# Kernel optimization log

Measured on AMD Instinct MI355X. Metric: run time of the kernel, lower is better.

The kernel has to match this reference:

```python
import jax, jax.numpy as jnp
from jax import lax
import numpy as np

T, B, D, H, A = 512, 2048, 64, 64, 16  # time, batch, input_dim, hidden_size, action_dim


def setup_inputs() -> dict:
    key = jax.random.key(0)
    ks = jax.random.split(key, 7)
    s = 1.0 / np.sqrt(H)  # PyTorch LSTMCell/Linear init scale
    return {
        "x": jax.random.normal(ks[0], (T, B, D), dtype=jnp.float32),
        "W_ih": jax.random.uniform(ks[1], (4 * H, D), jnp.float32, -s, s),
        "W_hh": jax.random.uniform(ks[2], (4 * H, H), jnp.float32, -s, s),
        "b_ih": jax.random.uniform(ks[3], (4 * H,), jnp.float32, -s, s),
        "b_hh": jax.random.uniform(ks[4], (4 * H,), jnp.float32, -s, s),
        "W_out": jax.random.uniform(ks[5], (A, H), jnp.float32, -s, s),
        "b_out": jax.random.uniform(ks[6], (A,), jnp.float32, -s, s),
    }


def reference(x, W_ih, W_hh, b_ih, b_hh, W_out, b_out):
    # x: [T, B, D]; single-layer LSTMCell unrolled over time via lax.scan,
    # zero initial (h, c) as in init_hidden_state(batch_size=B).
    Bh = x.shape[1]
    Hd = W_hh.shape[1]
    bias = b_ih + b_hh  # fuse the two biases

    def step(carry, x_t):
        h, c = carry
        gates = x_t @ W_ih.T + h @ W_hh.T + bias  # [B, 4H]
        i, f, g, o = jnp.split(gates, 4, axis=-1)  # PyTorch gate order i,f,g,o
        c_new = jax.nn.sigmoid(f) * c + jax.nn.sigmoid(i) * jnp.tanh(g)
        h_new = jax.nn.sigmoid(o) * jnp.tanh(c_new)
        return (h_new, c_new), h_new

    init = (jnp.zeros((Bh, Hd), x.dtype), jnp.zeros((Bh, Hd), x.dtype))
    _, hs = lax.scan(step, init, x)  # hs: [T, B, H]
    # 3D path applies network_out with NO nonlinearity, then stacks.
    return hs @ W_out.T + b_out  # [T, B, A]
```

## Files before the change

kernel.cpp:

```cpp
#include <hip/hip_runtime.h>
#include <hip/hip_bf16.h>


#define TT 512
#define BB 2048
#define DD 64
#define AA 16
#define ROWB 512

typedef short bf16x8 __attribute__((ext_vector_type(8)));
typedef float f32x4 __attribute__((ext_vector_type(4)));

#define MFMA16(a, b, c) __builtin_amdgcn_mfma_f32_16x16x32_bf16((a), (b), (c), 0, 0, 0)

#if defined(__has_builtin)
#  if __has_builtin(__builtin_amdgcn_exp2f)
#    define EXP2F(x) __builtin_amdgcn_exp2f(x)
#  else
#    define EXP2F(x) exp2f(x)
#  endif
#  if __has_builtin(__builtin_amdgcn_rcpf)
#    define RCPF(x) __builtin_amdgcn_rcpf(x)
#  else
#    define RCPF(x) (1.0f/(x))
#  endif
#else
#  define EXP2F(x) exp2f(x)
#  define RCPF(x) (1.0f/(x))
#endif

__device__ __forceinline__ float sigmoid_f(float x) {
  return RCPF(1.0f + EXP2F(-1.4426950408889634f * x));
}
__device__ __forceinline__ float tanh_f(float x) {
  return 1.0f - 2.0f * RCPF(1.0f + EXP2F(2.8853900817779268f * x));
}
__device__ __forceinline__ unsigned short bfu(float f) {
  union { __hip_bfloat16 b; unsigned short u; } cv;
  cv.b = __float2bfloat16(f);
  return cv.u;
}
__device__ __forceinline__ unsigned cvtpk2(float a, float b) {
  union { __hip_bfloat162 b2; unsigned u; } cv;
  cv.b2 = __float22bfloat162_rn(make_float2(a, b));
  return cv.u;
}
__device__ __forceinline__ float dpp_xor8(float v) {
  int i = __builtin_bit_cast(int, v);
  int r = __builtin_amdgcn_update_dpp(i, i, 0x128, 0xF, 0xF, true);
  return __builtin_bit_cast(float, r);
}
__device__ __forceinline__ int swz(int row, int slot) {
  return (slot ^ (row & 7) ^ ((row & 8) >> 1)) & 7;
}
__device__ __forceinline__ void block_sync_lds() {
  __builtin_amdgcn_sched_barrier(0);
  asm volatile("s_waitcnt lgkmcnt(0)" ::: "memory");
  __builtin_amdgcn_s_barrier();
  __builtin_amdgcn_sched_barrier(0);
}

__global__ __launch_bounds__(512, 2)
void lstm_actor_v10(const float* __restrict__ x,
                    const float* __restrict__ W_ih,
                    const float* __restrict__ W_hh,
                    const float* __restrict__ b_ih,
                    const float* __restrict__ b_hh,
                    const float* __restrict__ W_out,
                    const float* __restrict__ b_out,
                    float* __restrict__ out) {
  __shared__ __align__(16) unsigned short act[16 * ROWB / 2];
  char* actb = (char*)act;

  const int tid  = threadIdx.x;
  const int lane = tid & 63;
  const int w    = tid >> 6;
  const int lr   = lane & 15;
  const int lg   = lane >> 4;
  const int qq   = lr >> 3;
  const int jj   = lr & 7;
  const int r0   = blockIdx.x * 8;
  const int j0   = w * 8;

  const f32x4 Z = {0.f, 0.f, 0.f, 0.f};

  bf16x8 Bih[2][2], Bhh[2][2];
  float biasv[2];
#pragma unroll
  for (int nt = 0; nt < 2; ++nt) {
    const int g = (nt * 2 + qq) * 64 + j0 + jj;
    biasv[nt] = b_ih[g] + b_hh[g];
#pragma unroll
    for (int kt = 0; kt < 2; ++kt) {
      const float* si = W_ih + g * 64 + kt * 32 + lg * 8;
      const float* sh = W_hh + g * 64 + kt * 32 + lg * 8;
      bf16x8 vi, vh;
#pragma unroll
      for (int u = 0; u < 8; ++u) {
        vi[u] = (short)bfu(si[u]);
        vh[u] = (short)bfu(sh[u]);
      }
      Bih[nt][kt] = vi; Bhh[nt][kt] = vh;
    }
  }

  bf16x8 pb[2];
  const float bo = b_out[lr];
#pragma unroll
  for (int kt = 0; kt < 2; ++kt) {
    const float* src = W_out + lr * 64 + kt * 32 + lg * 8;
    bf16x8 vh;
#pragma unroll
    for (int u = 0; u < 8; ++u) vh[u] = (short)bfu(src[u]);
    pb[kt] = vh;
  }

  int aoffX[2], aoffH[2];
#pragma unroll
  for (int kt = 0; kt < 2; ++kt) {
    aoffX[kt] = lr * ROWB +       swz(lr, kt * 4 + lg) * 16;
    aoffH[kt] = lr * ROWB + 256 + swz(lr, kt * 4 + lg) * 16;
  }
  const int hrow = 2 * lg + qq;
  const int hj   = j0 + jj;
  const int hWb  = (2 * hrow) * ROWB + 256 + swz(2 * hrow, hj >> 3) * 16 + ((hj * 2) & 15);
  const int xrow = 2 * w + (lane >> 5);
  const int xj   = 2 * (lane & 31);
  const int xWb  = xrow * ROWB + swz(xrow, xj >> 3) * 16 + ((2 * xj) & 15);

  for (int i = tid; i < 16 * ROWB / 4; i += 512) ((unsigned*)act)[i] = 0u;
  __syncthreads();

  const float* xgl = x + (size_t)(r0 + w) * DD + xj + (size_t)(lane >> 5) * BB * DD;
  {
    const float2 v = *(const float2*)xgl;
    *(unsigned*)(actb + xWb) = cvtpk2(v.x, v.y);
  }
  float2 xw = *(const float2*)(xgl + (size_t)2 * BB * DD);
  float2 xf = *(const float2*)(xgl + (size_t)4 * BB * DD);
  xgl += (size_t)6 * BB * DD;

  float c_state = 0.0f;
  __syncthreads();

  f32x4 xCa, xCb;

  for (int it = 0; it < TT / 2; ++it) {
    const int xpR = (it & 1) << 7;
    const int xpW = 128 - xpR;

    {
      const int t = 2 * it;
      const bf16x8 A2 = *(const bf16x8*)(actb + aoffH[0]);
      const bf16x8 A3 = *(const bf16x8*)(actb + aoffH[1]);
      const bf16x8 X0 = *(const bf16x8*)(actb + aoffX[0] + xpR);
      const bf16x8 X1 = *(const bf16x8*)(actb + aoffX[1] + xpR);

      xCa = (f32x4){biasv[0], biasv[0], biasv[0], biasv[0]};
      xCb = (f32x4){biasv[1], biasv[1], biasv[1], biasv[1]};
      xCa = MFMA16(X0, Bih[0][0], xCa); xCa = MFMA16(X1, Bih[0][1], xCa);
      xCb = MFMA16(X0, Bih[1][0], xCb); xCb = MFMA16(X1, Bih[1][1], xCb);

      f32x4 H0 = MFMA16(A2, Bhh[0][0], Z); H0 = MFMA16(A3, Bhh[0][1], H0);
      f32x4 H1 = MFMA16(A2, Bhh[1][0], Z); H1 = MFMA16(A3, Bhh[1][1], H1);

      const bool do_proj = (w == (t & 7)) && (t > 0);
      f32x4 pacc = Z;
      if (do_proj) {
        pacc = MFMA16(A2, pb[0], Z);
        pacc = MFMA16(A3, pb[1], pacc);
      }

      const float a0 = H0[0] + xCa[0], b0 = H0[2] + xCa[2];
      const float a1 = H1[0] + xCb[0], b1 = H1[2] + xCb[2];
      const float rcv0 = dpp_xor8(qq ? a0 : b0);
      const float rcv1 = dpp_xor8(qq ? a1 : b1);
      const float iv_ = qq ? rcv0 : a0;
      const float fv_ = qq ? b0 : rcv0;
      const float gv_ = qq ? rcv1 : a1;
      const float ov_ = qq ? b1 : rcv1;

      const float iv = sigmoid_f(iv_);
      const float fv = sigmoid_f(fv_);
      const float gv = tanh_f(gv_);
      const float ov = sigmoid_f(ov_);
      c_state = fmaf(fv, c_state, iv * gv);
      const float h = ov * tanh_f(c_state);
      *(unsigned short*)(actb + hWb + 128) = bfu(h);

      *(unsigned*)(actb + xWb + xpW) = cvtpk2(xw.x, xw.y);
      xw = xf;
      if (it < TT / 2 - 3) xf = *(const float2*)xgl;
      xgl += (size_t)2 * BB * DD;

      if (do_proj) {
        const size_t base = ((size_t)(t - 1) * BB + r0 + 2 * lg) * AA + lr;
        out[base]      = pacc[0] + bo;
        out[base + AA] = pacc[2] + bo;
      }
      block_sync_lds();
    }

    {
      const int t = 2 * it + 1;
      const bf16x8 A2 = *(const bf16x8*)(actb + aoffH[0] + 128);
      const bf16x8 A3 = *(const bf16x8*)(actb + aoffH[1] + 128);

      f32x4 H0 = MFMA16(A2, Bhh[0][0], Z); H0 = MFMA16(A3, Bhh[0][1], H0);
      f32x4 H1 = MFMA16(A2, Bhh[1][0], Z); H1 = MFMA16(A3, Bhh[1][1], H1);

      const bool do_proj = (w == (t & 7));
      f32x4 pacc = Z;
      if (do_proj) {
        pacc = MFMA16(A2, pb[0], Z);
        pacc = MFMA16(A3, pb[1], pacc);
      }

      const float a0 = H0[0] + xCa[1], b0 = H0[2] + xCa[3];
      const float a1 = H1[0] + xCb[1], b1 = H1[2] + xCb[3];
      const float rcv0 = dpp_xor8(qq ? a0 : b0);
      const float rcv1 = dpp_xor8(qq ? a1 : b1);
      const float iv_ = qq ? rcv0 : a0;
      const float fv_ = qq ? b0 : rcv0;
      const float gv_ = qq ? rcv1 : a1;
      const float ov_ = qq ? b1 : rcv1;

      const float iv = sigmoid_f(iv_);
      const float fv = sigmoid_f(fv_);
      const float gv = tanh_f(gv_);
      const float ov = sigmoid_f(ov_);
      c_state = fmaf(fv, c_state, iv * gv);
      const float h = ov * tanh_f(c_state);
      *(unsigned short*)(actb + hWb) = bfu(h);

      if (do_proj) {
        const size_t base = ((size_t)(t - 1) * BB + r0 + 2 * lg) * AA + lr;
        out[base]      = pacc[0] + bo;
        out[base + AA] = pacc[2] + bo;
      }
      block_sync_lds();
    }
  }

  if (w == (TT & 7)) {
    const bf16x8 A2 = *(const bf16x8*)(actb + aoffH[0]);
    const bf16x8 A3 = *(const bf16x8*)(actb + aoffH[1]);
    f32x4 pacc = MFMA16(A2, pb[0], Z);
    pacc = MFMA16(A3, pb[1], pacc);
    const size_t base = ((size_t)(TT - 1) * BB + r0 + 2 * lg) * AA + lr;
    out[base]      = pacc[0] + bo;
    out[base + AA] = pacc[2] + bo;
  }
}

extern "C" void kernel_launch(void* const* d_in, const int* in_sizes, int n_in,
                              void* d_out, int out_size, void* d_ws, size_t ws_size,
                              hipStream_t stream) {
  const float* x     = (const float*)d_in[0];
  const float* W_ih  = (const float*)d_in[1];
  const float* W_hh  = (const float*)d_in[2];
  const float* b_ih  = (const float*)d_in[3];
  const float* b_hh  = (const float*)d_in[4];
  const float* W_out = (const float*)d_in[5];
  const float* b_out = (const float*)d_in[6];
  float* out = (float*)d_out;

  lstm_actor_v10<<<dim3(BB / 8), dim3(512), 0, stream>>>(
      x, W_ih, W_hh, b_ih, b_hh, W_out, b_out, out);
}
```

Measured before the change: 213.1 us.

## Prefetch x-projection one step ahead and fold gate activation scales into weights

The input projection MFMA for the next pair of timesteps is now computed one step early, in the odd step, and ping-ponged between two accumulator sets. The recurrent MFMAs then accumulate directly onto it, taking that work off the critical dependency chain at each step. The sigmoid and tanh pre-scaling constants are folded into the bf16 weights and biases so the per-step activation math drops a multiply. The LDS row layout shrinks to 384 bytes with a different swizzle and separate h buffers. Folding the scales into weights before bf16 rounding slightly changes numerics.

```diff
diff --git a/kernel.cpp b/kernel.cpp
--- a/kernel.cpp
+++ b/kernel.cpp
@@ -6,7 +6,7 @@
 #define BB 2048
 #define DD 64
 #define AA 16
-#define ROWB 512
+#define ROWB 384
 
 typedef short bf16x8 __attribute__((ext_vector_type(8)));
 typedef float f32x4 __attribute__((ext_vector_type(4)));
@@ -29,12 +29,9 @@
 #  define RCPF(x) (1.0f/(x))
 #endif
 
-__device__ __forceinline__ float sigmoid_f(float x) {
-  return RCPF(1.0f + EXP2F(-1.4426950408889634f * x));
-}
-__device__ __forceinline__ float tanh_f(float x) {
-  return 1.0f - 2.0f * RCPF(1.0f + EXP2F(2.8853900817779268f * x));
-}
+#define GS_I (-1.4426950408889634f)
+#define GS_G (2.8853900817779268f)
+
 __device__ __forceinline__ unsigned short bfu(float f) {
   union { __hip_bfloat16 b; unsigned short u; } cv;
   cv.b = __float2bfloat16(f);
@@ -51,7 +48,7 @@
   return __builtin_bit_cast(float, r);
 }
 __device__ __forceinline__ int swz(int row, int slot) {
-  return (slot ^ (row & 7) ^ ((row & 8) >> 1)) & 7;
+  return (slot ^ (row & 7) ^ ((row & 8) >> 3)) & 7;
 }
 __device__ __forceinline__ void block_sync_lds() {
   __builtin_amdgcn_sched_barrier(0);
@@ -61,14 +58,14 @@
 }
 
 __global__ __launch_bounds__(512, 2)
-void lstm_actor_v10(const float* __restrict__ x,
-                    const float* __restrict__ W_ih,
-                    const float* __restrict__ W_hh,
-                    const float* __restrict__ b_ih,
-                    const float* __restrict__ b_hh,
-                    const float* __restrict__ W_out,
-                    const float* __restrict__ b_out,
-                    float* __restrict__ out) {
+void lstm_actor_v11b(const float* __restrict__ x,
+                     const float* __restrict__ W_ih,
+                     const float* __restrict__ W_hh,
+                     const float* __restrict__ b_ih,
+                     const float* __restrict__ b_hh,
+                     const float* __restrict__ W_out,
+                     const float* __restrict__ b_out,
+                     float* __restrict__ out) {
   __shared__ __align__(16) unsigned short act[16 * ROWB / 2];
   char* actb = (char*)act;
 
@@ -89,7 +86,8 @@
 #pragma unroll
   for (int nt = 0; nt < 2; ++nt) {
     const int g = (nt * 2 + qq) * 64 + j0 + jj;
-    biasv[nt] = b_ih[g] + b_hh[g];
+    const float sc = (nt == 1 && qq == 0) ? GS_G : GS_I;
+    biasv[nt] = sc * (b_ih[g] + b_hh[g]);
 #pragma unroll
     for (int kt = 0; kt < 2; ++kt) {
       const float* si = W_ih + g * 64 + kt * 32 + lg * 8;
@@ -97,8 +95,8 @@
       bf16x8 vi, vh;
 #pragma unroll
       for (int u = 0; u < 8; ++u) {
-        vi[u] = (short)bfu(si[u]);
-        vh[u] = (short)bfu(sh[u]);
+        vi[u] = (short)bfu(sc * si[u]);
+        vh[u] = (short)bfu(sc * sh[u]);
       }
       Bih[nt][kt] = vi; Bhh[nt][kt] = vh;
     }
@@ -115,15 +113,16 @@
     pb[kt] = vh;
   }
 
-  int aoffX[2], aoffH[2];
+  int aoffX[2], aoffH0[2], aoffH1[2];
 #pragma unroll
   for (int kt = 0; kt < 2; ++kt) {
-    aoffX[kt] = lr * ROWB +       swz(lr, kt * 4 + lg) * 16;
-    aoffH[kt] = lr * ROWB + 256 + swz(lr, kt * 4 + lg) * 16;
+    aoffX[kt]  = lr * ROWB + swz(lr, kt * 4 + lg) * 16;
+    aoffH0[kt] = aoffX[kt] + 128;
+    aoffH1[kt] = aoffX[kt] + 256;
   }
   const int hrow = 2 * lg + qq;
-  const int hj   = j0 + jj;
-  const int hWb  = (2 * hrow) * ROWB + 256 + swz(2 * hrow, hj >> 3) * 16 + ((hj * 2) & 15);
+  const int hW0 = (2 * hrow) * ROWB + 128 + swz(2 * hrow, w) * 16 + 2 * jj;
+  const int hW1 = (2 * hrow + 1) * ROWB + 256 + swz(2 * hrow + 1, w) * 16 + 2 * jj;
   const int xrow = 2 * w + (lane >> 5);
   const int xj   = 2 * (lane & 31);
   const int xWb  = xrow * ROWB + swz(xrow, xj >> 3) * 16 + ((2 * xj) & 15);
@@ -139,112 +138,89 @@
   float2 xw = *(const float2*)(xgl + (size_t)2 * BB * DD);
   float2 xf = *(const float2*)(xgl + (size_t)4 * BB * DD);
   xgl += (size_t)6 * BB * DD;
-
+  __syncthreads();
+
+  f32x4 xPa = {biasv[0], biasv[0], biasv[0], biasv[0]};
+  f32x4 xPb = {biasv[1], biasv[1], biasv[1], biasv[1]};
+  {
+    const bf16x8 X0 = *(const bf16x8*)(actb + aoffX[0]);
+    const bf16x8 X1 = *(const bf16x8*)(actb + aoffX[1]);
+    xPa = MFMA16(X0, Bih[0][0], xPa); xPa = MFMA16(X1, Bih[0][1], xPa);
+    xPb = MFMA16(X0, Bih[1][0], xPb); xPb = MFMA16(X1, Bih[1][1], xPb);
+  }
+  f32x4 xQa = Z, xQb = Z;
   float c_state = 0.0f;
-  __syncthreads();
-
-  f32x4 xCa, xCb;
-
-  for (int it = 0; it < TT / 2; ++it) {
-    const int xpR = (it & 1) << 7;
-    const int xpW = 128 - xpR;
-
-    {
-      const int t = 2 * it;
-      const bf16x8 A2 = *(const bf16x8*)(actb + aoffH[0]);
-      const bf16x8 A3 = *(const bf16x8*)(actb + aoffH[1]);
-      const bf16x8 X0 = *(const bf16x8*)(actb + aoffX[0] + xpR);
-      const bf16x8 X1 = *(const bf16x8*)(actb + aoffX[1] + xpR);
-
-      xCa = (f32x4){biasv[0], biasv[0], biasv[0], biasv[0]};
-      xCb = (f32x4){biasv[1], biasv[1], biasv[1], biasv[1]};
-      xCa = MFMA16(X0, Bih[0][0], xCa); xCa = MFMA16(X1, Bih[0][1], xCa);
-      xCb = MFMA16(X0, Bih[1][0], xCb); xCb = MFMA16(X1, Bih[1][1], xCb);
-
-      f32x4 H0 = MFMA16(A2, Bhh[0][0], Z); H0 = MFMA16(A3, Bhh[0][1], H0);
-      f32x4 H1 = MFMA16(A2, Bhh[1][0], Z); H1 = MFMA16(A3, Bhh[1][1], H1);
-
-      const bool do_proj = (w == (t & 7)) && (t > 0);
-      f32x4 pacc = Z;
-      if (do_proj) {
-        pacc = MFMA16(A2, pb[0], Z);
-        pacc = MFMA16(A3, pb[1], pacc);
-      }
-
-      const float a0 = H0[0] + xCa[0], b0 = H0[2] + xCa[2];
-      const float a1 = H1[0] + xCb[0], b1 = H1[2] + xCb[2];
-      const float rcv0 = dpp_xor8(qq ? a0 : b0);
-      const float rcv1 = dpp_xor8(qq ? a1 : b1);
-      const float iv_ = qq ? rcv0 : a0;
-      const float fv_ = qq ? b0 : rcv0;
-      const float gv_ = qq ? rcv1 : a1;
-      const float ov_ = qq ? b1 : rcv1;
-
-      const float iv = sigmoid_f(iv_);
-      const float fv = sigmoid_f(fv_);
-      const float gv = tanh_f(gv_);
-      const float ov = sigmoid_f(ov_);
-      c_state = fmaf(fv, c_state, iv * gv);
-      const float h = ov * tanh_f(c_state);
-      *(unsigned short*)(actb + hWb + 128) = bfu(h);
-
-      *(unsigned*)(actb + xWb + xpW) = cvtpk2(xw.x, xw.y);
-      xw = xf;
-      if (it < TT / 2 - 3) xf = *(const float2*)xgl;
-      xgl += (size_t)2 * BB * DD;
-
-      if (do_proj) {
-        const size_t base = ((size_t)(t - 1) * BB + r0 + 2 * lg) * AA + lr;
-        out[base]      = pacc[0] + bo;
-        out[base + AA] = pacc[2] + bo;
-      }
-      block_sync_lds();
+  block_sync_lds();
+
+  auto gates_and_h = [&](float a0, float b0, float a1, float b1, int hWoff) {
+    const float rcv0 = dpp_xor8(qq ? a0 : b0);
+    const float rcv1 = dpp_xor8(qq ? a1 : b1);
+    const float iv_ = qq ? rcv0 : a0;
+    const float fv_ = qq ? b0 : rcv0;
+    const float gv_ = qq ? rcv1 : a1;
+    const float ov_ = qq ? b1 : rcv1;
+    const float iv = RCPF(1.0f + EXP2F(iv_));
+    const float fv = RCPF(1.0f + EXP2F(fv_));
+    const float gv = fmaf(-2.0f, RCPF(1.0f + EXP2F(gv_)), 1.0f);
+    const float ov = RCPF(1.0f + EXP2F(ov_));
+    c_state = fmaf(fv, c_state, iv * gv);
+    const float tc = fmaf(-2.0f, RCPF(1.0f + EXP2F(GS_G * c_state)), 1.0f);
+    *(unsigned short*)(actb + hWoff) = bfu(ov * tc);
+  };
+  auto proj = [&](int t, int tmod, int sel, const bf16x8& A2, const bf16x8& A3) {
+    if (w == tmod && t > 0) {
+      f32x4 pacc = MFMA16(A2, pb[0], Z);
+      pacc = MFMA16(A3, pb[1], pacc);
+      const size_t base = ((size_t)(t - 1) * BB + r0 + 2 * lg) * AA + lr;
+      out[base]      = pacc[sel]     + bo;
+      out[base + AA] = pacc[sel + 2] + bo;
     }
-
-    {
-      const int t = 2 * it + 1;
-      const bf16x8 A2 = *(const bf16x8*)(actb + aoffH[0] + 128);
-      const bf16x8 A3 = *(const bf16x8*)(actb + aoffH[1] + 128);
-
-      f32x4 H0 = MFMA16(A2, Bhh[0][0], Z); H0 = MFMA16(A3, Bhh[0][1], H0);
-      f32x4 H1 = MFMA16(A2, Bhh[1][0], Z); H1 = MFMA16(A3, Bhh[1][1], H1);
-
-      const bool do_proj = (w == (t & 7));
-      f32x4 pacc = Z;
-      if (do_proj) {
-        pacc = MFMA16(A2, pb[0], Z);
-        pacc = MFMA16(A3, pb[1], pacc);
-      }
-
-      const float a0 = H0[0] + xCa[1], b0 = H0[2] + xCa[3];
-      const float a1 = H1[0] + xCb[1], b1 = H1[2] + xCb[3];
-      const float rcv0 = dpp_xor8(qq ? a0 : b0);
-      const float rcv1 = dpp_xor8(qq ? a1 : b1);
-      const float iv_ = qq ? rcv0 : a0;
-      const float fv_ = qq ? b0 : rcv0;
-      const float gv_ = qq ? rcv1 : a1;
-      const float ov_ = qq ? b1 : rcv1;
-
-      const float iv = sigmoid_f(iv_);
-      const float fv = sigmoid_f(fv_);
-      const float gv = tanh_f(gv_);
-      const float ov = sigmoid_f(ov_);
-      c_state = fmaf(fv, c_state, iv * gv);
-      const float h = ov * tanh_f(c_state);
-      *(unsigned short*)(actb + hWb) = bfu(h);
-
-      if (do_proj) {
-        const size_t base = ((size_t)(t - 1) * BB + r0 + 2 * lg) * AA + lr;
-        out[base]      = pacc[0] + bo;
-        out[base + AA] = pacc[2] + bo;
-      }
-      block_sync_lds();
-    }
+  };
+  auto stepA = [&](int t, int tmod, const f32x4& ca, const f32x4& cb) {
+    const bf16x8 A2 = *(const bf16x8*)(actb + aoffH0[0]);
+    const bf16x8 A3 = *(const bf16x8*)(actb + aoffH0[1]);
+    f32x4 H0 = MFMA16(A2, Bhh[0][0], ca); H0 = MFMA16(A3, Bhh[0][1], H0);
+    f32x4 H1 = MFMA16(A2, Bhh[1][0], cb); H1 = MFMA16(A3, Bhh[1][1], H1);
+    proj(t, tmod, 0, A2, A3);
+    *(unsigned*)(actb + xWb) = cvtpk2(xw.x, xw.y);
+    xw = xf;
+    if (t + 7 < TT) xf = *(const float2*)xgl;
+    xgl += (size_t)2 * BB * DD;
+    gates_and_h(H0[0], H0[2], H1[0], H1[2], hW1);
+    block_sync_lds();
+  };
+  auto stepB = [&](int t, int tmod, const f32x4& ca, const f32x4& cb,
+                   f32x4& na, f32x4& nb) {
+    const bf16x8 A2 = *(const bf16x8*)(actb + aoffH1[0]);
+    const bf16x8 A3 = *(const bf16x8*)(actb + aoffH1[1]);
+    const bf16x8 X0 = *(const bf16x8*)(actb + aoffX[0]);
+    const bf16x8 X1 = *(const bf16x8*)(actb + aoffX[1]);
+    f32x4 H0 = MFMA16(A2, Bhh[0][0], ca); H0 = MFMA16(A3, Bhh[0][1], H0);
+    f32x4 H1 = MFMA16(A2, Bhh[1][0], cb); H1 = MFMA16(A3, Bhh[1][1], H1);
+    na = (f32x4){biasv[0], biasv[0], biasv[0], biasv[0]};
+    nb = (f32x4){biasv[1], biasv[1], biasv[1], biasv[1]};
+    na = MFMA16(X0, Bih[0][0], na); na = MFMA16(X1, Bih[0][1], na);
+    nb = MFMA16(X0, Bih[1][0], nb); nb = MFMA16(X1, Bih[1][1], nb);
+    proj(t, tmod, 1, A2, A3);
+    gates_and_h(H0[1], H0[3], H1[1], H1[3], hW0);
+    block_sync_lds();
+  };
+
+  for (int u = 0; u < TT / 8; ++u) {
+    const int t0 = u * 8;
+    stepA(t0 + 0, 0, xPa, xPb);
+    stepB(t0 + 1, 1, xPa, xPb, xQa, xQb);
+    stepA(t0 + 2, 2, xQa, xQb);
+    stepB(t0 + 3, 3, xQa, xQb, xPa, xPb);
+    stepA(t0 + 4, 4, xPa, xPb);
+    stepB(t0 + 5, 5, xPa, xPb, xQa, xQb);
+    stepA(t0 + 6, 6, xQa, xQb);
+    stepB(t0 + 7, 7, xQa, xQb, xPa, xPb);
   }
 
   if (w == (TT & 7)) {
-    const bf16x8 A2 = *(const bf16x8*)(actb + aoffH[0]);
-    const bf16x8 A3 = *(const bf16x8*)(actb + aoffH[1]);
+    const bf16x8 A2 = *(const bf16x8*)(actb + aoffH0[0]);
+    const bf16x8 A3 = *(const bf16x8*)(actb + aoffH0[1]);
     f32x4 pacc = MFMA16(A2, pb[0], Z);
     pacc = MFMA16(A3, pb[1], pacc);
     const size_t base = ((size_t)(TT - 1) * BB + r0 + 2 * lg) * AA + lr;
@@ -265,6 +241,6 @@
   const float* b_out = (const float*)d_in[6];
   float* out = (float*)d_out;
 
-  lstm_actor_v10<<<dim3(BB / 8), dim3(512), 0, stream>>>(
+  lstm_actor_v11b<<<dim3(BB / 8), dim3(512), 0, stream>>>(
       x, W_ih, W_hh, b_ih, b_hh, W_out, b_out, out);
 }
```

Measured after the change: 244.1 us. 1.15x slower.
